# Kernel tuning notes

Measured on AMD Instinct MI355X. Metric: run time of the kernel, lower is better.

## Reference

```python
import jax, jax.numpy as jnp
import numpy as np

B, C, H, W = 8, 64, 64, 64
CQK = C // 8

def setup_inputs() -> dict:
    key = jax.random.key(0)
    ks = jax.random.split(key, 8)
    s = 0.05
    return {
        "X": jax.random.normal(ks[0], (B, C, H, W), dtype=jnp.float32),
        "Wq": jax.random.normal(ks[1], (CQK, C), dtype=jnp.float32) * s,
        "bq": jax.random.normal(ks[2], (CQK,), dtype=jnp.float32) * s,
        "Wk": jax.random.normal(ks[3], (CQK, C), dtype=jnp.float32) * s,
        "bk": jax.random.normal(ks[4], (CQK,), dtype=jnp.float32) * s,
        "Wv": jax.random.normal(ks[5], (C, C), dtype=jnp.float32) * s,
        "bv": jax.random.normal(ks[6], (C,), dtype=jnp.float32) * s,
        "gamma": jax.random.normal(ks[7], (1,), dtype=jnp.float32) * 0.5,
    }

def reference(X, Wq, bq, Wk, bk, Wv, bv, gamma):
    b, c, h, w = X.shape
    n = h * w
    Xf = X.reshape(b, c, n)  # [B, C, N]
    # 1x1 convs == per-pixel linear over channels
    q = jnp.einsum('oc,bcn->bno', Wq, Xf) + bq            # [B, N, Cqk]
    k = jnp.einsum('oc,bcn->bon', Wk, Xf) + bk[:, None]    # [B, Cqk, N]
    v = jnp.einsum('oc,bcn->bon', Wv, Xf) + bv[:, None]    # [B, C, N]
    energy = jnp.einsum('bnd,bdm->bnm', q, k)              # [B, N, N] (no scale, as in source)
    attention = jax.nn.softmax(energy, axis=-1)
    out = jnp.einsum('bcn,bmn->bcm', v, attention)         # value @ attention^T
    out = out.reshape(b, c, h, w)
    return X + out * gamma[0]
```

## Files before the change

kernel.cpp:

```cpp
#include <hip/hip_runtime.h>
#include <hip/hip_bf16.h>

#define BB 8
#define CC 64
#define NN 4096
#define LOG2E 1.44269504088896340736f

typedef short bf16x8 __attribute__((ext_vector_type(8)));
typedef float f32x16 __attribute__((ext_vector_type(16)));
typedef unsigned int uint4v __attribute__((ext_vector_type(4)));

__device__ __forceinline__ unsigned cvt_pk_bf16(float lo, float hi) {
    unsigned r;
    asm("v_cvt_pk_bf16_f32 %0, %1, %2" : "=v"(r) : "v"(lo), "v"(hi));
    return r;
}

__device__ __forceinline__ float fast_exp2(float x) {
    int i = (int)__builtin_fmaf(x, 8388608.f, 1064992087.f);
    return __builtin_bit_cast(float, i);
}


__global__ __launch_bounds__(256) void qkv_kernel(
    const float* __restrict__ X,
    const float* __restrict__ Wq, const float* __restrict__ bq,
    const float* __restrict__ Wk, const float* __restrict__ bk,
    const float* __restrict__ Wv, const float* __restrict__ bv,
    unsigned short* __restrict__ qw, unsigned short* __restrict__ kfrag,
    unsigned short* __restrict__ vfrag)
{
    __shared__ float wbuf[64 * 16];
    __shared__ float bsh[16];
    __shared__ short vsh[16][264];

    const int t = threadIdx.x;
    const int grp = blockIdx.x % 5;
    const int tile = blockIdx.x / 5;
    const int b = tile >> 4;
    const int nb = (tile & 15) << 8;
    const int n = nb + t;

    if (grp == 0) {
        for (int i = t; i < 512; i += 256) {
            int o = i >> 6, c = i & 63;
            wbuf[c * 16 + o]     = Wq[i];
            wbuf[c * 16 + 8 + o] = Wk[i];
        }
        if (t < 8) { bsh[t] = bq[t]; bsh[8 + t] = bk[t]; }
    } else {
        const int cbase = (grp - 1) * 16;
        for (int i = t; i < 1024; i += 256) {
            int o = i >> 6, c = i & 63;
            wbuf[c * 16 + o] = Wv[(cbase + o) * 64 + c];
        }
        if (t < 16) bsh[t] = bv[cbase + t];
    }
    __syncthreads();

    float a[16];
    #pragma unroll
    for (int j = 0; j < 16; j++) a[j] = bsh[j];

    const float* xp = X + (size_t)b * CC * NN + n;
    for (int c = 0; c < 64; c++) {
        float xc = xp[(size_t)c * NN];
        const float4* w4 = (const float4*)&wbuf[c * 16];
        float4 w0 = w4[0], w1 = w4[1], w2 = w4[2], w3 = w4[3];
        a[0]  += w0.x * xc; a[1]  += w0.y * xc; a[2]  += w0.z * xc; a[3]  += w0.w * xc;
        a[4]  += w1.x * xc; a[5]  += w1.y * xc; a[6]  += w1.z * xc; a[7]  += w1.w * xc;
        a[8]  += w2.x * xc; a[9]  += w2.y * xc; a[10] += w2.z * xc; a[11] += w2.w * xc;
        a[12] += w3.x * xc; a[13] += w3.y * xc; a[14] += w3.z * xc; a[15] += w3.w * xc;
    }

    if (grp == 0) {
        alignas(16) __hip_bfloat16 qb8[8], kb8[8];
        #pragma unroll
        for (int d = 0; d < 8; d++) {
            qb8[d] = __float2bfloat16(a[d] * LOG2E);
            kb8[d] = __float2bfloat16(a[8 + d]);
        }
        const size_t g = (size_t)b * NN + n;
        *(int4*)(qw + g * 8) = *(const int4*)qb8;
        size_t kf = ((size_t)b * 128 + (n >> 5)) * 512;
        *(int4*)(kfrag + kf + (size_t)(n & 31) * 8) = *(const int4*)kb8;
        *(int4*)(kfrag + kf + (size_t)(32 + (n & 31)) * 8) = make_int4(0, 0, 0, 0);
    } else {
        const int cbase = (grp - 1) * 16;
        const int qb0 = cbase & 31, ct = cbase >> 5;
        #pragma unroll
        for (int j = 0; j < 16; j++)
            vsh[j][t] = __builtin_bit_cast(short, __float2bfloat16(a[j]));
        __syncthreads();
        #pragma unroll
        for (int rr = 0; rr < 2; ++rr) {
            int r = 2 * t + rr;
            int qq = r & 15, hh = (r >> 4) & 1, gg = (r >> 5) & 3, tau = r >> 7;
            int n0 = tau * 64 + gg * 16 + hh * 8;
            int4 val = *(const int4*)&vsh[qq][n0];
            int gtile = (nb >> 6) + tau;
            size_t dst = ((size_t)(b * 64 + gtile)) * 4096
                       + (size_t)(gg * 2 + ct) * 512
                       + (size_t)(32 * hh + qb0 + qq) * 8;
            *(int4*)(vfrag + dst) = val;
        }
    }
}

template<int KS, bool FUSE>
__global__ __launch_bounds__(256, 2) void attn_kernel(
    const unsigned short* __restrict__ qw,
    const unsigned short* __restrict__ kfrag,
    const unsigned short* __restrict__ vfrag,
    unsigned short* __restrict__ pout, float* __restrict__ pl,
    const float* __restrict__ X, const float* __restrict__ gamma,
    float* __restrict__ out)
{
    const int t = threadIdx.x;
    const int w = t >> 6, lane = t & 63;
    const int h = lane >> 5, q = lane & 31;

    const int nwg = gridDim.x;
    const int cpx = nwg >> 3;
    const int bid = (blockIdx.x & 7) * cpx + (blockIdx.x >> 3);

    const int qtile = bid & 15;
    const int b = (bid >> 4) & 7;
    const int ks = bid >> 7;

    const int qbase = qtile * 256 + w * 64;

    bf16x8 qfA = {}, qfB = {};
    if (h == 0) {
        qfA = *(const bf16x8*)(qw + ((size_t)b * NN + qbase + q) * 8);
        qfB = *(const bf16x8*)(qw + ((size_t)b * NN + qbase + 32 + q) * 8);
    }

    f32x16 accA0 = {}, accA1 = {}, accB0 = {}, accB1 = {};
    float lsumA = 0.f, lsumB = 0.f;

    const int NT = NN / KS / 64;
    const unsigned short* kb = kfrag + (size_t)b * 65536
                             + (size_t)ks * NT * 1024 + (size_t)lane * 8;
    const unsigned short* vbp = vfrag + (size_t)b * 262144
                              + (size_t)ks * NT * 4096 + (size_t)lane * 8;

    auto phase = [&](const f32x16& sA, const f32x16& sB,
                     bf16x8 va, bf16x8 vb2, bf16x8 vc, bf16x8 vd) {
        float pa[16], pb[16];
        #pragma unroll
        for (int r = 0; r < 16; ++r) { pa[r] = fast_exp2(sA[r]); pb[r] = fast_exp2(sB[r]); }
        {
            float a0 = 0.f, a1 = 0.f, b0 = 0.f, b1 = 0.f;
            #pragma unroll
            for (int r = 0; r < 8; ++r) {
                a0 += pa[r]; a1 += pa[8 + r];
                b0 += pb[r]; b1 += pb[8 + r];
            }
            lsumA += a0 + a1;
            lsumB += b0 + b1;
        }
        unsigned ka[8], kb2[8];
        #pragma unroll
        for (int j = 0; j < 8; ++j) {
            ka[j]  = cvt_pk_bf16(pa[2 * j], pa[2 * j + 1]);
            kb2[j] = cvt_pk_bf16(pb[2 * j], pb[2 * j + 1]);
        }
        __builtin_amdgcn_s_setprio(1);
        #pragma unroll
        for (int g2 = 0; g2 < 2; ++g2) {
            const unsigned* pga = &ka[4 * g2];
            auto ra = __builtin_amdgcn_permlane32_swap(pga[2], pga[0], false, false);
            auto rb = __builtin_amdgcn_permlane32_swap(pga[3], pga[1], false, false);
            uint4v bua = { ra[1], rb[1], ra[0], rb[0] };
            bf16x8 pfA = __builtin_bit_cast(bf16x8, bua);
            const unsigned* pgb = &kb2[4 * g2];
            auto rc = __builtin_amdgcn_permlane32_swap(pgb[2], pgb[0], false, false);
            auto rd = __builtin_amdgcn_permlane32_swap(pgb[3], pgb[1], false, false);
            uint4v bub = { rc[1], rd[1], rc[0], rd[0] };
            bf16x8 pfB = __builtin_bit_cast(bf16x8, bub);

            bf16x8 vx = g2 ? vc : va;
            bf16x8 vy = g2 ? vd : vb2;
            accA0 = __builtin_amdgcn_mfma_f32_32x32x16_bf16(vx, pfA, accA0, 0, 0, 0);
            accA1 = __builtin_amdgcn_mfma_f32_32x32x16_bf16(vy, pfA, accA1, 0, 0, 0);
            accB0 = __builtin_amdgcn_mfma_f32_32x32x16_bf16(vx, pfB, accB0, 0, 0, 0);
            accB1 = __builtin_amdgcn_mfma_f32_32x32x16_bf16(vy, pfB, accB1, 0, 0, 0);
        }
        __builtin_amdgcn_s_setprio(0);
    };

    bf16x8 kc0 = *(const bf16x8*)kb;
    bf16x8 kc1 = *(const bf16x8*)(kb + 512);

    for (int it = 0; it < NT; ++it) {
        const unsigned short* vp = vbp + (size_t)it * 4096;
        bf16x8 v0 = *(const bf16x8*)(vp);
        bf16x8 v1 = *(const bf16x8*)(vp + 512);
        bf16x8 v2 = *(const bf16x8*)(vp + 1024);
        bf16x8 v3 = *(const bf16x8*)(vp + 1536);
        bf16x8 v4 = *(const bf16x8*)(vp + 2048);
        bf16x8 v5 = *(const bf16x8*)(vp + 2560);
        bf16x8 v6 = *(const bf16x8*)(vp + 3072);
        bf16x8 v7 = *(const bf16x8*)(vp + 3584);

        const int nit = (it + 1 < NT) ? it + 1 : it;
        const unsigned short* knp = kb + (size_t)nit * 1024;
        bf16x8 kn0 = *(const bf16x8*)knp;
        bf16x8 kn1 = *(const bf16x8*)(knp + 512);

        {
            f32x16 sA = __builtin_amdgcn_mfma_f32_32x32x16_bf16(kc0, qfA, (f32x16){}, 0, 0, 0);
            f32x16 sB = __builtin_amdgcn_mfma_f32_32x32x16_bf16(kc0, qfB, (f32x16){}, 0, 0, 0);
            phase(sA, sB, v0, v1, v2, v3);
        }
        {
            f32x16 sA = __builtin_amdgcn_mfma_f32_32x32x16_bf16(kc1, qfA, (f32x16){}, 0, 0, 0);
            f32x16 sB = __builtin_amdgcn_mfma_f32_32x32x16_bf16(kc1, qfB, (f32x16){}, 0, 0, 0);
            phase(sA, sB, v4, v5, v6, v7);
        }
        kc0 = kn0;
        kc1 = kn1;
    }

    auto rsA = __builtin_amdgcn_permlane32_swap(__builtin_bit_cast(unsigned, lsumA),
                                                __builtin_bit_cast(unsigned, lsumA), false, false);
    float ltotA = __builtin_bit_cast(float, rsA[0]) + __builtin_bit_cast(float, rsA[1]);
    auto rsB = __builtin_amdgcn_permlane32_swap(__builtin_bit_cast(unsigned, lsumB),
                                                __builtin_bit_cast(unsigned, lsumB), false, false);
    float ltotB = __builtin_bit_cast(float, rsB[0]) + __builtin_bit_cast(float, rsB[1]);

    const float gm = FUSE ? gamma[0] : 0.f;

    #pragma unroll
    for (int sub = 0; sub < 2; ++sub) {
        const int n = qbase + sub * 32 + q;
        const float ltot = sub ? ltotB : ltotA;
        const f32x16& a0 = sub ? accB0 : accA0;
        const f32x16& a1 = sub ? accB1 : accA1;
        if (FUSE) {
            const float inv = 1.f / ltot;
            #pragma unroll
            for (int ct = 0; ct < 2; ++ct) {
                const f32x16& a = ct ? a1 : a0;
                #pragma unroll
                for (int r = 0; r < 16; ++r) {
                    int c = ct * 32 + (r & 3) + 8 * (r >> 2) + 4 * h;
                    size_t idx = ((size_t)(b * CC + c)) * NN + n;
                    out[idx] = X[idx] + gm * a[r] * inv;
                }
            }
        } else {
            unsigned short* po = pout + (size_t)ks * BB * CC * NN;
            #pragma unroll
            for (int ct = 0; ct < 2; ++ct) {
                const f32x16& a = ct ? a1 : a0;
                #pragma unroll
                for (int r = 0; r < 16; ++r) {
                    int c = ct * 32 + (r & 3) + 8 * (r >> 2) + 4 * h;
                    po[((size_t)(b * CC + c)) * NN + n] =
                        __builtin_bit_cast(unsigned short, __float2bfloat16(a[r]));
                }
            }
            if (h == 0) pl[((size_t)(ks * BB + b)) * NN + n] = ltot;
        }
    }
}

template<int KS>
__global__ __launch_bounds__(256) void combine_kernel(
    const unsigned short* __restrict__ pout, const float* __restrict__ pl,
    const float* __restrict__ X, const float* __restrict__ gamma,
    float* __restrict__ out)
{
    const int idx = blockIdx.x * 256 + threadIdx.x;
    const int n4 = idx & 1023;
    const int c  = (idx >> 10) & 63;
    const int b  = idx >> 16;
    const int n0 = n4 * 4;
    const float gm = gamma[0];
    const size_t base = ((size_t)(b * CC + c)) * NN + n0;

    float4 s = make_float4(0.f, 0.f, 0.f, 0.f);
    float4 L = make_float4(0.f, 0.f, 0.f, 0.f);
    #pragma unroll
    for (int ks = 0; ks < KS; ++ks) {
        ushort4 sv = *(const ushort4*)(pout + (size_t)ks * BB * CC * NN + base);
        float4 lv = *(const float4*)(pl + ((size_t)(ks * BB + b)) * NN + n0);
        s.x += __bfloat162float(__builtin_bit_cast(__hip_bfloat16, sv.x));
        s.y += __bfloat162float(__builtin_bit_cast(__hip_bfloat16, sv.y));
        s.z += __bfloat162float(__builtin_bit_cast(__hip_bfloat16, sv.z));
        s.w += __bfloat162float(__builtin_bit_cast(__hip_bfloat16, sv.w));
        L.x += lv.x; L.y += lv.y; L.z += lv.z; L.w += lv.w;
    }
    float4 x = *(const float4*)(X + base);
    float4 o;
    o.x = x.x + gm * s.x / L.x;
    o.y = x.y + gm * s.y / L.y;
    o.z = x.z + gm * s.z / L.z;
    o.w = x.w + gm * s.w / L.w;
    *(float4*)(out + base) = o;
}

extern "C" void kernel_launch(void* const* d_in, const int* in_sizes, int n_in,
                              void* d_out, int out_size, void* d_ws, size_t ws_size,
                              hipStream_t stream) {
    const float* X  = (const float*)d_in[0];
    const float* Wq = (const float*)d_in[1];
    const float* bq = (const float*)d_in[2];
    const float* Wk = (const float*)d_in[3];
    const float* bk = (const float*)d_in[4];
    const float* Wv = (const float*)d_in[5];
    const float* bv = (const float*)d_in[6];
    const float* gm = (const float*)d_in[7];
    float* out = (float*)d_out;

    unsigned short* qw    = (unsigned short*)d_ws;
    unsigned short* kfrag = qw + (size_t)BB * NN * 8;
    unsigned short* vfrag = kfrag + (size_t)BB * 128 * 512;
    unsigned short* pout  = vfrag + (size_t)BB * 64 * 4096;
    float* pl = (float*)(pout + (size_t)8 * BB * CC * NN);

    const size_t qkv_bytes = ((size_t)BB * NN * 8 + (size_t)BB * 128 * 512
                            + (size_t)BB * 64 * 4096) * 2;
    const size_t need8 = qkv_bytes + (size_t)8 * BB * CC * NN * 2 + (size_t)8 * BB * NN * 4;
    const size_t need4 = qkv_bytes + (size_t)4 * BB * CC * NN * 2 + (size_t)4 * BB * NN * 4;

    qkv_kernel<<<dim3(640), dim3(256), 0, stream>>>(X, Wq, bq, Wk, bk, Wv, bv, qw, kfrag, vfrag);

    if (ws_size >= need8) {
        attn_kernel<8, false><<<dim3(1024), dim3(256), 0, stream>>>(
            qw, kfrag, vfrag, pout, pl, X, gm, out);
        combine_kernel<8><<<dim3((BB * CC * NN / 4) / 256), dim3(256), 0, stream>>>(
            pout, pl, X, gm, out);
    } else if (ws_size >= need4) {
        float* pl4 = (float*)(pout + (size_t)4 * BB * CC * NN);
        attn_kernel<4, false><<<dim3(512), dim3(256), 0, stream>>>(
            qw, kfrag, vfrag, pout, pl4, X, gm, out);
        combine_kernel<4><<<dim3((BB * CC * NN / 4) / 256), dim3(256), 0, stream>>>(
            pout, pl4, X, gm, out);
    } else {
        attn_kernel<1, true><<<dim3(128), dim3(256), 0, stream>>>(
            qw, kfrag, vfrag, nullptr, nullptr, X, gm, out);
    }
}
```

Baseline: 57.09 us.

## Stage K/V tiles through double-buffered LDS via global_load_lds

Each attention block now cooperatively loads the K and V fragment tiles into double-buffered shared memory with direct global-to-LDS loads, so the next tile is prefetched while the current one is computed. Before, each of the 4 waves loaded the same K/V tiles from global memory itself. The aim is to cut redundant global/L2 traffic and hide load latency. In exchange it adds two block barriers per iteration, explicit vmcnt waits, and LDS usage that could lower occupancy.

```diff
diff --git a/kernel.cpp b/kernel.cpp
--- a/kernel.cpp
+++ b/kernel.cpp
@@ -19,6 +19,17 @@
 __device__ __forceinline__ float fast_exp2(float x) {
     int i = (int)__builtin_fmaf(x, 8388608.f, 1064992087.f);
     return __builtin_bit_cast(float, i);
+}
+
+__device__ __forceinline__ void vmwait3()  { asm volatile("s_waitcnt vmcnt(3)" ::: "memory"); }
+__device__ __forceinline__ void vmwait2()  { asm volatile("s_waitcnt vmcnt(2)" ::: "memory"); }
+__device__ __forceinline__ void vmwait0()  { asm volatile("s_waitcnt vmcnt(0)" ::: "memory"); }
+__device__ __forceinline__ void lgkmwait0(){ asm volatile("s_waitcnt lgkmcnt(0)" ::: "memory"); }
+
+__device__ __forceinline__ void glds16(const void* g, void* l) {
+    __builtin_amdgcn_global_load_lds(
+        (const __attribute__((address_space(1))) unsigned int*)g,
+        (__attribute__((address_space(3))) unsigned int*)l, 16, 0, 0);
 }
 
 
@@ -116,6 +127,9 @@
     const float* __restrict__ X, const float* __restrict__ gamma,
     float* __restrict__ out)
 {
+    __shared__ alignas(16) short klds[2][1024];
+    __shared__ alignas(16) short vlds[2][4096];
+
     const int t = threadIdx.x;
     const int w = t >> 6, lane = t & 63;
     const int h = lane >> 5, q = lane & 31;
@@ -140,13 +154,22 @@
     float lsumA = 0.f, lsumB = 0.f;
 
     const int NT = NN / KS / 64;
-    const unsigned short* kb = kfrag + (size_t)b * 65536
-                             + (size_t)ks * NT * 1024 + (size_t)lane * 8;
-    const unsigned short* vbp = vfrag + (size_t)b * 262144
-                              + (size_t)ks * NT * 4096 + (size_t)lane * 8;
-
-    auto phase = [&](const f32x16& sA, const f32x16& sB,
-                     bf16x8 va, bf16x8 vb2, bf16x8 vc, bf16x8 vd) {
+    const int t0 = ks * NT;
+
+    auto stage = [&](int buf, int gt) {
+        const unsigned short* vsrc = vfrag + ((size_t)(b * 64 + gt)) * 4096;
+        short* vdst = &vlds[buf][0];
+        glds16(vsrc + (size_t)w * 512 + (size_t)lane * 8,       vdst + (size_t)w * 512);
+        glds16(vsrc + (size_t)(w + 4) * 512 + (size_t)lane * 8, vdst + (size_t)(w + 4) * 512);
+        if (w < 2) {
+            const unsigned short* ksrc = kfrag + ((size_t)b * 128 + (size_t)gt * 2 + w) * 512;
+            glds16(ksrc + (size_t)lane * 8, &klds[buf][w * 512]);
+        }
+    };
+
+    auto phase = [&](bf16x8 kc, bf16x8 va, bf16x8 vb2, bf16x8 vc, bf16x8 vd) {
+        f32x16 sA = __builtin_amdgcn_mfma_f32_32x32x16_bf16(kc, qfA, (f32x16){}, 0, 0, 0);
+        f32x16 sB = __builtin_amdgcn_mfma_f32_32x32x16_bf16(kc, qfB, (f32x16){}, 0, 0, 0);
         float pa[16], pb[16];
         #pragma unroll
         for (int r = 0; r < 16; ++r) { pa[r] = fast_exp2(sA[r]); pb[r] = fast_exp2(sB[r]); }
@@ -179,7 +202,6 @@
             auto rd = __builtin_amdgcn_permlane32_swap(pgb[3], pgb[1], false, false);
             uint4v bub = { rc[1], rd[1], rc[0], rd[0] };
             bf16x8 pfB = __builtin_bit_cast(bf16x8, bub);
-
             bf16x8 vx = g2 ? vc : va;
             bf16x8 vy = g2 ? vd : vb2;
             accA0 = __builtin_amdgcn_mfma_f32_32x32x16_bf16(vx, pfA, accA0, 0, 0, 0);
@@ -190,37 +212,37 @@
         __builtin_amdgcn_s_setprio(0);
     };
 
-    bf16x8 kc0 = *(const bf16x8*)kb;
-    bf16x8 kc1 = *(const bf16x8*)(kb + 512);
+    stage(0, t0);
 
     for (int it = 0; it < NT; ++it) {
-        const unsigned short* vp = vbp + (size_t)it * 4096;
-        bf16x8 v0 = *(const bf16x8*)(vp);
-        bf16x8 v1 = *(const bf16x8*)(vp + 512);
-        bf16x8 v2 = *(const bf16x8*)(vp + 1024);
-        bf16x8 v3 = *(const bf16x8*)(vp + 1536);
-        bf16x8 v4 = *(const bf16x8*)(vp + 2048);
-        bf16x8 v5 = *(const bf16x8*)(vp + 2560);
-        bf16x8 v6 = *(const bf16x8*)(vp + 3072);
-        bf16x8 v7 = *(const bf16x8*)(vp + 3584);
-
-        const int nit = (it + 1 < NT) ? it + 1 : it;
-        const unsigned short* knp = kb + (size_t)nit * 1024;
-        bf16x8 kn0 = *(const bf16x8*)knp;
-        bf16x8 kn1 = *(const bf16x8*)(knp + 512);
-
-        {
-            f32x16 sA = __builtin_amdgcn_mfma_f32_32x32x16_bf16(kc0, qfA, (f32x16){}, 0, 0, 0);
-            f32x16 sB = __builtin_amdgcn_mfma_f32_32x32x16_bf16(kc0, qfB, (f32x16){}, 0, 0, 0);
-            phase(sA, sB, v0, v1, v2, v3);
-        }
-        {
-            f32x16 sA = __builtin_amdgcn_mfma_f32_32x32x16_bf16(kc1, qfA, (f32x16){}, 0, 0, 0);
-            f32x16 sB = __builtin_amdgcn_mfma_f32_32x32x16_bf16(kc1, qfB, (f32x16){}, 0, 0, 0);
-            phase(sA, sB, v4, v5, v6, v7);
-        }
-        kc0 = kn0;
-        kc1 = kn1;
+        const int cur = it & 1;
+        if (it + 1 < NT) {
+            stage(cur ^ 1, t0 + it + 1);
+            if (w < 2) vmwait3(); else vmwait2();
+        } else {
+            vmwait0();
+        }
+        __builtin_amdgcn_s_barrier();
+        __builtin_amdgcn_sched_barrier(0);
+
+        const short* kl = &klds[cur][0];
+        const short* vl = &vlds[cur][0];
+        bf16x8 kc0 = *(const bf16x8*)(kl + (size_t)lane * 8);
+        bf16x8 kc1 = *(const bf16x8*)(kl + 512 + (size_t)lane * 8);
+        bf16x8 v0 = *(const bf16x8*)(vl + (size_t)lane * 8);
+        bf16x8 v1 = *(const bf16x8*)(vl + 512 + (size_t)lane * 8);
+        bf16x8 v2 = *(const bf16x8*)(vl + 1024 + (size_t)lane * 8);
+        bf16x8 v3 = *(const bf16x8*)(vl + 1536 + (size_t)lane * 8);
+        bf16x8 v4 = *(const bf16x8*)(vl + 2048 + (size_t)lane * 8);
+        bf16x8 v5 = *(const bf16x8*)(vl + 2560 + (size_t)lane * 8);
+        bf16x8 v6 = *(const bf16x8*)(vl + 3072 + (size_t)lane * 8);
+        bf16x8 v7 = *(const bf16x8*)(vl + 3584 + (size_t)lane * 8);
+
+        phase(kc0, v0, v1, v2, v3);
+        phase(kc1, v4, v5, v6, v7);
+
+        lgkmwait0();
+        __builtin_amdgcn_s_barrier();
     }
 
     auto rsA = __builtin_amdgcn_permlane32_swap(__builtin_bit_cast(unsigned, lsumA),
```

Measured after the change: 57.71 us. Within noise of the previous version (+1.1%).

## Prefetch V fragments one iteration ahead and drop the 8-way key split

Applied to the files above, without the earlier changes.

The attention loop now loads the next iteration's V fragments alongside the next K fragments, double-buffering them in registers. A sched_barrier keeps the prefetch loads ahead of the compute. The host also removes the 8-way key-split path, so the 4-way split with 512 blocks is the default. This hides global load latency for V and shrinks the partial-output traffic the combine kernel reads, but it raises register pressure and halves the grid size.

```diff
diff --git a/kernel.cpp b/kernel.cpp
--- a/kernel.cpp
+++ b/kernel.cpp
@@ -145,8 +145,9 @@
     const unsigned short* vbp = vfrag + (size_t)b * 262144
                               + (size_t)ks * NT * 4096 + (size_t)lane * 8;
 
-    auto phase = [&](const f32x16& sA, const f32x16& sB,
-                     bf16x8 va, bf16x8 vb2, bf16x8 vc, bf16x8 vd) {
+    auto phase = [&](bf16x8 kc, bf16x8 va, bf16x8 vb2, bf16x8 vc, bf16x8 vd) {
+        f32x16 sA = __builtin_amdgcn_mfma_f32_32x32x16_bf16(kc, qfA, (f32x16){}, 0, 0, 0);
+        f32x16 sB = __builtin_amdgcn_mfma_f32_32x32x16_bf16(kc, qfB, (f32x16){}, 0, 0, 0);
         float pa[16], pb[16];
         #pragma unroll
         for (int r = 0; r < 16; ++r) { pa[r] = fast_exp2(sA[r]); pb[r] = fast_exp2(sB[r]); }
@@ -179,7 +180,6 @@
             auto rd = __builtin_amdgcn_permlane32_swap(pgb[3], pgb[1], false, false);
             uint4v bub = { rc[1], rd[1], rc[0], rd[0] };
             bf16x8 pfB = __builtin_bit_cast(bf16x8, bub);
-
             bf16x8 vx = g2 ? vc : va;
             bf16x8 vy = g2 ? vd : vb2;
             accA0 = __builtin_amdgcn_mfma_f32_32x32x16_bf16(vx, pfA, accA0, 0, 0, 0);
@@ -192,35 +192,37 @@
 
     bf16x8 kc0 = *(const bf16x8*)kb;
     bf16x8 kc1 = *(const bf16x8*)(kb + 512);
+    bf16x8 vc0 = *(const bf16x8*)(vbp);
+    bf16x8 vc1 = *(const bf16x8*)(vbp + 512);
+    bf16x8 vc2 = *(const bf16x8*)(vbp + 1024);
+    bf16x8 vc3 = *(const bf16x8*)(vbp + 1536);
+    bf16x8 vc4 = *(const bf16x8*)(vbp + 2048);
+    bf16x8 vc5 = *(const bf16x8*)(vbp + 2560);
+    bf16x8 vc6 = *(const bf16x8*)(vbp + 3072);
+    bf16x8 vc7 = *(const bf16x8*)(vbp + 3584);
 
     for (int it = 0; it < NT; ++it) {
-        const unsigned short* vp = vbp + (size_t)it * 4096;
-        bf16x8 v0 = *(const bf16x8*)(vp);
-        bf16x8 v1 = *(const bf16x8*)(vp + 512);
-        bf16x8 v2 = *(const bf16x8*)(vp + 1024);
-        bf16x8 v3 = *(const bf16x8*)(vp + 1536);
-        bf16x8 v4 = *(const bf16x8*)(vp + 2048);
-        bf16x8 v5 = *(const bf16x8*)(vp + 2560);
-        bf16x8 v6 = *(const bf16x8*)(vp + 3072);
-        bf16x8 v7 = *(const bf16x8*)(vp + 3584);
-
         const int nit = (it + 1 < NT) ? it + 1 : it;
         const unsigned short* knp = kb + (size_t)nit * 1024;
+        const unsigned short* vnp = vbp + (size_t)nit * 4096;
         bf16x8 kn0 = *(const bf16x8*)knp;
         bf16x8 kn1 = *(const bf16x8*)(knp + 512);
-
-        {
-            f32x16 sA = __builtin_amdgcn_mfma_f32_32x32x16_bf16(kc0, qfA, (f32x16){}, 0, 0, 0);
-            f32x16 sB = __builtin_amdgcn_mfma_f32_32x32x16_bf16(kc0, qfB, (f32x16){}, 0, 0, 0);
-            phase(sA, sB, v0, v1, v2, v3);
-        }
-        {
-            f32x16 sA = __builtin_amdgcn_mfma_f32_32x32x16_bf16(kc1, qfA, (f32x16){}, 0, 0, 0);
-            f32x16 sB = __builtin_amdgcn_mfma_f32_32x32x16_bf16(kc1, qfB, (f32x16){}, 0, 0, 0);
-            phase(sA, sB, v4, v5, v6, v7);
-        }
-        kc0 = kn0;
-        kc1 = kn1;
+        bf16x8 vn0 = *(const bf16x8*)(vnp);
+        bf16x8 vn1 = *(const bf16x8*)(vnp + 512);
+        bf16x8 vn2 = *(const bf16x8*)(vnp + 1024);
+        bf16x8 vn3 = *(const bf16x8*)(vnp + 1536);
+        bf16x8 vn4 = *(const bf16x8*)(vnp + 2048);
+        bf16x8 vn5 = *(const bf16x8*)(vnp + 2560);
+        bf16x8 vn6 = *(const bf16x8*)(vnp + 3072);
+        bf16x8 vn7 = *(const bf16x8*)(vnp + 3584);
+        __builtin_amdgcn_sched_barrier(0);
+
+        phase(kc0, vc0, vc1, vc2, vc3);
+        phase(kc1, vc4, vc5, vc6, vc7);
+
+        kc0 = kn0; kc1 = kn1;
+        vc0 = vn0; vc1 = vn1; vc2 = vn2; vc3 = vn3;
+        vc4 = vn4; vc5 = vn5; vc6 = vn6; vc7 = vn7;
     }
 
     auto rsA = __builtin_amdgcn_permlane32_swap(__builtin_bit_cast(unsigned, lsumA),
@@ -319,26 +321,19 @@
     unsigned short* kfrag = qw + (size_t)BB * NN * 8;
     unsigned short* vfrag = kfrag + (size_t)BB * 128 * 512;
     unsigned short* pout  = vfrag + (size_t)BB * 64 * 4096;
-    float* pl = (float*)(pout + (size_t)8 * BB * CC * NN);
+    float* pl = (float*)(pout + (size_t)4 * BB * CC * NN);
 
     const size_t qkv_bytes = ((size_t)BB * NN * 8 + (size_t)BB * 128 * 512
                             + (size_t)BB * 64 * 4096) * 2;
-    const size_t need8 = qkv_bytes + (size_t)8 * BB * CC * NN * 2 + (size_t)8 * BB * NN * 4;
     const size_t need4 = qkv_bytes + (size_t)4 * BB * CC * NN * 2 + (size_t)4 * BB * NN * 4;
 
     qkv_kernel<<<dim3(640), dim3(256), 0, stream>>>(X, Wq, bq, Wk, bk, Wv, bv, qw, kfrag, vfrag);
 
-    if (ws_size >= need8) {
-        attn_kernel<8, false><<<dim3(1024), dim3(256), 0, stream>>>(
+    if (ws_size >= need4) {
+        attn_kernel<4, false><<<dim3(512), dim3(256), 0, stream>>>(
             qw, kfrag, vfrag, pout, pl, X, gm, out);
-        combine_kernel<8><<<dim3((BB * CC * NN / 4) / 256), dim3(256), 0, stream>>>(
+        combine_kernel<4><<<dim3((BB * CC * NN / 4) / 256), dim3(256), 0, stream>>>(
             pout, pl, X, gm, out);
-    } else if (ws_size >= need4) {
-        float* pl4 = (float*)(pout + (size_t)4 * BB * CC * NN);
-        attn_kernel<4, false><<<dim3(512), dim3(256), 0, stream>>>(
-            qw, kfrag, vfrag, pout, pl4, X, gm, out);
-        combine_kernel<4><<<dim3((BB * CC * NN / 4) / 256), dim3(256), 0, stream>>>(
-            pout, pl4, X, gm, out);
     } else {
         attn_kernel<1, true><<<dim3(128), dim3(256), 0, stream>>>(
             qw, kfrag, vfrag, nullptr, nullptr, X, gm, out);
```

Result: faster. 53.45 us (-6.4%).
